# Optimization experiments

Measured on AMD Instinct MI355X. Metric: run time of the kernel, lower is better.

Reference implementation:

```python
import jax, jax.numpy as jnp
import numpy as np

B, S, D, H = 8, 8192, 256, 256


def setup_inputs() -> dict:
    key = jax.random.key(0)
    ks = jax.random.split(key, 5)
    scale = 1.0 / np.sqrt(D)  # mimic nn.Linear init scale
    return {
        "x": jax.random.normal(ks[0], (B, S, D), dtype=jnp.float32),
        "h0": jnp.zeros((B, 1, H), dtype=jnp.float32),
        "w_h_w": jax.random.normal(ks[1], (H, D), dtype=jnp.float32) * scale,
        "w_h_b": jax.random.normal(ks[2], (H,), dtype=jnp.float32) * scale,
        "w_z_w": jax.random.normal(ks[3], (H, D), dtype=jnp.float32) * scale,
        "w_z_b": jax.random.normal(ks[4], (H,), dtype=jnp.float32) * scale,
    }


def reference(x, h0, w_h_w, w_h_b, w_z_w, w_z_b):
    # Projections over the whole sequence (same math as per-step Linear calls)
    z = jax.nn.sigmoid(jnp.einsum('bsd,hd->bsh', x, w_z_w) + w_z_b)  # [B,S,H]
    h_tilde = jnp.einsum('bsd,hd->bsh', x, w_h_w) + w_h_b            # [B,S,H]

    def step(h_prev, zh):
        z_t, ht_t = zh  # each [B,H]
        h_t = (1.0 - z_t) * h_prev + z_t * ht_t
        return h_t, h_t

    # scan over time axis; carry is [B,H]
    _, hs = jax.lax.scan(step, h0[:, 0],
                         (jnp.swapaxes(z, 0, 1), jnp.swapaxes(h_tilde, 0, 1)))
    return jnp.swapaxes(hs, 0, 1)  # [B,S,H]
```

## Files before the change

### kernel.cpp

```cpp
#include <hip/hip_runtime.h>
#include <math.h>


constexpr int B_ = 8;
constexpr int S_ = 8192;
constexpr int D_ = 256;
constexpr int H_ = 256;
constexpr int M_ = B_ * S_;
constexpr int CHUNKS = 128;
constexpr int CLEN = S_ / CHUNKS;

typedef __attribute__((ext_vector_type(8))) short bf16x8;
typedef __attribute__((ext_vector_type(4))) float f32x4;

__device__ __forceinline__ uint pack2bf(float f0, float f1) {
  const uint u0 = __float_as_uint(f0) + 0x8000u;
  const uint u1 = __float_as_uint(f1) + 0x8000u;
  return __builtin_amdgcn_perm(u1, u0, 0x07060302u);
}

__device__ __forceinline__ float a_of(uint u) { return __uint_as_float(u << 16); }
__device__ __forceinline__ float b_of(uint u) { return __uint_as_float(u & 0xFFFF0000u); }

__global__ __launch_bounds__(256) void prep_w(
    const float* __restrict__ wzw, const float* __restrict__ whw,
    uint4* __restrict__ wb)
{
  const int u = blockIdx.x * 256 + threadIdx.x;
  const int proj = u >> 13;
  const float* s = (proj ? whw : wzw) + (size_t)(u & 8191) * 8;
  wb[u] = make_uint4(pack2bf(s[0], s[1]), pack2bf(s[2], s[3]),
                     pack2bf(s[4], s[5]), pack2bf(s[6], s[7]));
}

__global__ __launch_bounds__(512, 4) void gemm_zh(
    const float* __restrict__ x, const ushort* __restrict__ wbu,
    const float* __restrict__ whb, const float* __restrict__ wzb,
    uint* __restrict__ ab, float2* __restrict__ chunkPQ)
{
  __shared__ ushort xs[128][72];
  __shared__ ushort wzs[128][72];
  __shared__ ushort whs[128][72];

  const int tid = threadIdx.x;
  const int g    = blockIdx.x;
  const int xcd  = g & 7;
  const int loc  = g >> 3;
  const int nt   = loc & 1;
  const int panel = (loc >> 1) * 8 + xcd;
  const int m0 = panel * 128;
  const int n0 = nt * 128;

  const int lane = tid & 63;
  const int w  = tid >> 6;
  const int mb = (w & 1) * 64;
  const int nb = (w >> 1) * 32;
  const int q  = lane >> 4;
  const int cn = lane & 15;

  f32x4 accz[4][2] = {};
  f32x4 acch[4][2] = {};

  for (int k0 = 0; k0 < D_; k0 += 64) {
    __syncthreads();
#pragma unroll
    for (int f = 0; f < 4; f++) {
      const int idx = tid + 512 * f;
      const int row = idx >> 4, seg = idx & 15;
      float4 v = *(const float4*)(x + (size_t)(m0 + row) * D_ + k0 + seg * 4);
      *(uint2*)&xs[row][seg * 4] =
          make_uint2(pack2bf(v.x, v.y), pack2bf(v.z, v.w));
    }
#pragma unroll
    for (int f = 0; f < 4; f++) {
      const int idx = tid + 512 * f;
      const int proj = idx >> 10;
      const int r   = (idx >> 3) & 127, seg = idx & 7;
      const uint4 v = *(const uint4*)(wbu + (size_t)proj * H_ * D_ +
                                      (size_t)(n0 + r) * D_ + k0 + seg * 8);
      ushort* dst = proj ? &whs[r][seg * 8] : &wzs[r][seg * 8];
      *(uint4*)dst = v;
    }
    __syncthreads();
#pragma unroll
    for (int ks = 0; ks < 2; ks++) {
      const int kk = ks * 32 + q * 8;
      bf16x8 af[4], bz[2], bh[2];
#pragma unroll
      for (int i = 0; i < 4; i++)
        af[i] = *(const bf16x8*)&xs[mb + i * 16 + cn][kk];
#pragma unroll
      for (int j = 0; j < 2; j++) {
        bz[j] = *(const bf16x8*)&wzs[nb + j * 16 + cn][kk];
        bh[j] = *(const bf16x8*)&whs[nb + j * 16 + cn][kk];
      }
#pragma unroll
      for (int i = 0; i < 4; i++)
#pragma unroll
        for (int j = 0; j < 2; j++) {
          accz[i][j] = __builtin_amdgcn_mfma_f32_16x16x32_bf16(af[i], bz[j], accz[i][j], 0, 0, 0);
          acch[i][j] = __builtin_amdgcn_mfma_f32_16x16x32_bf16(af[i], bh[j], acch[i][j], 0, 0, 0);
        }
    }
  }

  const int row0 = m0 + mb;
  const int bb2  = row0 >> 13;
  const int cc   = (row0 & 8191) >> 6;

#pragma unroll
  for (int j = 0; j < 2; j++) {
    const int ch = n0 + nb + j * 16 + cn;
    const float zb = wzb[ch], hb = whb[ch];
    uint u[4][4];
#pragma unroll
    for (int i = 0; i < 4; i++) {
#pragma unroll
      for (int r = 0; r < 4; r++) {
        const int row = m0 + mb + i * 16 + q * 4 + r;
        const float zpre = accz[i][j][r] + zb;
        const float hpre = acch[i][j][r] + hb;
        const float e = __expf(-zpre);
        const float rcp = __builtin_amdgcn_rcpf(1.0f + e);
        const uint pk = pack2bf(e * rcp, hpre * rcp);
        ab[(size_t)row * H_ + ch] = pk;
        u[i][r] = pk;
      }
    }
    float P[4], Q[4];
#pragma unroll
    for (int i = 0; i < 4; i++) {
      float Pi = 1.f, Qi = 0.f;
#pragma unroll
      for (int r = 0; r < 4; r++) {
        const float a  = a_of(u[i][r]);
        const float bv = b_of(u[i][r]);
        Qi = fmaf(a, Qi, bv);
        Pi *= a;
      }
      P[i] = Pi; Q[i] = Qi;
    }
#pragma unroll
    for (int i = 0; i < 4; i++) {
      {
        const float Pp = __shfl_xor(P[i], 16);
        const float Qp = __shfl_xor(Q[i], 16);
        const bool later = (lane & 16) != 0;
        Q[i] = later ? fmaf(P[i], Qp, Q[i]) : fmaf(Pp, Q[i], Qp);
        P[i] = P[i] * Pp;
      }
      {
        const float Pp = __shfl_xor(P[i], 32);
        const float Qp = __shfl_xor(Q[i], 32);
        const bool later = (lane & 32) != 0;
        Q[i] = later ? fmaf(P[i], Qp, Q[i]) : fmaf(Pp, Q[i], Qp);
        P[i] = P[i] * Pp;
      }
    }
    float Pc = P[0], Qc = Q[0];
#pragma unroll
    for (int i = 1; i < 4; i++) {
      Qc = fmaf(P[i], Qc, Q[i]);
      Pc *= P[i];
    }
    if (lane < 16)
      chunkPQ[((size_t)bb2 * CHUNKS + cc) * H_ + ch] = make_float2(Pc, Qc);
  }
}

__global__ __launch_bounds__(256) void scan_phaseB(
    const float* __restrict__ h0in, const float2* __restrict__ pq,
    float* __restrict__ hstate)
{
  const int b = blockIdx.x;
  const int h = threadIdx.x;
  const size_t base = (size_t)b * CHUNKS * H_ + h;
  float hc = h0in[(size_t)b * H_ + h];
  for (int c0 = 0; c0 < CHUNKS; c0 += 16) {
    float2 v[16];
#pragma unroll
    for (int j = 0; j < 16; j++)
      v[j] = pq[base + (size_t)(c0 + j) * H_];
#pragma unroll
    for (int j = 0; j < 16; j++) {
      hstate[base + (size_t)(c0 + j) * H_] = hc;
      hc = fmaf(v[j].x, hc, v[j].y);
    }
  }
}

__global__ __launch_bounds__(64) void scan_phaseC(
    const uint* __restrict__ ab, const float* __restrict__ hstate,
    float* __restrict__ out)
{
  const int cid = blockIdx.x;
  const int b = cid >> 7;
  const int c = cid & (CHUNKS - 1);
  const int ch4 = threadIdx.x * 4;
  const size_t ebase = ((size_t)b * S_ + (size_t)c * CLEN) * H_ + ch4;

  float4 h4 = *(const float4*)(hstate + ((size_t)b * CHUNKS + c) * H_ + ch4);
  float h0v = h4.x, h1v = h4.y, h2v = h4.z, h3v = h4.w;

#pragma unroll
  for (int t0 = 0; t0 < CLEN; t0 += 8) {
    uint4 v[8];
#pragma unroll
    for (int j = 0; j < 8; j++)
      v[j] = *(const uint4*)(ab + ebase + (size_t)(t0 + j) * H_);
#pragma unroll
    for (int j = 0; j < 8; j++) {
      float4 o;
      o.x = h0v = fmaf(a_of(v[j].x), h0v, b_of(v[j].x));
      o.y = h1v = fmaf(a_of(v[j].y), h1v, b_of(v[j].y));
      o.z = h2v = fmaf(a_of(v[j].z), h2v, b_of(v[j].z));
      o.w = h3v = fmaf(a_of(v[j].w), h3v, b_of(v[j].w));
      *(float4*)(out + ebase + (size_t)(t0 + j) * H_) = o;
    }
  }
}

extern "C" void kernel_launch(void* const* d_in, const int* in_sizes, int n_in,
                              void* d_out, int out_size, void* d_ws, size_t ws_size,
                              hipStream_t stream) {
  const float* x   = (const float*)d_in[0];
  const float* h0  = (const float*)d_in[1];
  const float* whw = (const float*)d_in[2];
  const float* whb = (const float*)d_in[3];
  const float* wzw = (const float*)d_in[4];
  const float* wzb = (const float*)d_in[5];
  float* out = (float*)d_out;

  uint*   ab      = (uint*)d_ws;
  float2* chunkPQ = (float2*)(ab + (size_t)M_ * H_);
  float*  hstate  = (float*)(chunkPQ + (size_t)B_ * CHUNKS * H_);
  ushort* wb      = (ushort*)(hstate + (size_t)B_ * CHUNKS * H_);

  prep_w<<<64, 256, 0, stream>>>(wzw, whw, (uint4*)wb);
  gemm_zh<<<(M_ / 128) * (H_ / 128), 512, 0, stream>>>(
      x, wb, whb, wzb, ab, chunkPQ);
  scan_phaseB<<<B_, 256, 0, stream>>>(h0, (const float2*)chunkPQ, hstate);
  scan_phaseC<<<B_ * CHUNKS, 64, 0, stream>>>(ab, hstate, out);
}
```

Baseline: 177.2 us.

## Split scan phase C into four sub-chunks using per-sub-chunk carry products

The GEMM epilogue now also stores the per-16-row (P,Q) partial composites for each 64-step chunk. Phase C launches four wavefronts per chunk: each one first advances the chunk's starting state through the preceding sub-chunks, then scans only its own 16 timesteps. This cuts the serial dependency length per thread by four and raises parallelism in the memory-bound final pass. The cost is an extra partial-product buffer written by the GEMM and read by phase C, plus a few extra FMAs per thread.

```diff
diff --git a/kernel.cpp b/kernel.cpp
--- a/kernel.cpp
+++ b/kernel.cpp
@@ -36,7 +36,8 @@
 __global__ __launch_bounds__(512, 4) void gemm_zh(
     const float* __restrict__ x, const ushort* __restrict__ wbu,
     const float* __restrict__ whb, const float* __restrict__ wzb,
-    uint* __restrict__ ab, float2* __restrict__ chunkPQ)
+    uint* __restrict__ ab, float2* __restrict__ chunkPQ,
+    float2* __restrict__ pqsub)
 {
   __shared__ ushort xs[128][72];
   __shared__ ushort wzs[128][72];
@@ -112,9 +113,10 @@
   for (int j = 0; j < 2; j++) {
     const int ch = n0 + nb + j * 16 + cn;
     const float zb = wzb[ch], hb = whb[ch];
-    uint u[4][4];
+    float P[4], Q[4];
 #pragma unroll
     for (int i = 0; i < 4; i++) {
+      float Pi = 1.f, Qi = 0.f;
 #pragma unroll
       for (int r = 0; r < 4; r++) {
         const int row = m0 + mb + i * 16 + q * 4 + r;
@@ -124,17 +126,8 @@
         const float rcp = __builtin_amdgcn_rcpf(1.0f + e);
         const uint pk = pack2bf(e * rcp, hpre * rcp);
         ab[(size_t)row * H_ + ch] = pk;
-        u[i][r] = pk;
-      }
-    }
-    float P[4], Q[4];
-#pragma unroll
-    for (int i = 0; i < 4; i++) {
-      float Pi = 1.f, Qi = 0.f;
-#pragma unroll
-      for (int r = 0; r < 4; r++) {
-        const float a  = a_of(u[i][r]);
-        const float bv = b_of(u[i][r]);
+        const float a  = a_of(pk);
+        const float bv = b_of(pk);
         Qi = fmaf(a, Qi, bv);
         Pi *= a;
       }
@@ -163,8 +156,13 @@
       Qc = fmaf(P[i], Qc, Q[i]);
       Pc *= P[i];
     }
-    if (lane < 16)
+    if (lane < 16) {
+      const size_t sb = ((size_t)bb2 * CHUNKS + cc) * 4;
+#pragma unroll
+      for (int i = 0; i < 4; i++)
+        pqsub[(sb + i) * H_ + ch] = make_float2(P[i], Q[i]);
       chunkPQ[((size_t)bb2 * CHUNKS + cc) * H_ + ch] = make_float2(Pc, Qc);
+    }
   }
 }
 
@@ -189,21 +187,38 @@
   }
 }
 
-__global__ __launch_bounds__(64) void scan_phaseC(
+__global__ __launch_bounds__(256) void scan_phaseC(
     const uint* __restrict__ ab, const float* __restrict__ hstate,
-    float* __restrict__ out)
+    const float2* __restrict__ pqsub, float* __restrict__ out)
 {
   const int cid = blockIdx.x;
   const int b = cid >> 7;
   const int c = cid & (CHUNKS - 1);
-  const int ch4 = threadIdx.x * 4;
-  const size_t ebase = ((size_t)b * S_ + (size_t)c * CLEN) * H_ + ch4;
+  const int g = threadIdx.x >> 6;
+  const int ch4 = (threadIdx.x & 63) * 4;
 
   float4 h4 = *(const float4*)(hstate + ((size_t)b * CHUNKS + c) * H_ + ch4);
   float h0v = h4.x, h1v = h4.y, h2v = h4.z, h3v = h4.w;
 
-#pragma unroll
-  for (int t0 = 0; t0 < CLEN; t0 += 8) {
+  const float2* ps = pqsub + ((size_t)b * CHUNKS + c) * 4 * H_ + ch4;
+#pragma unroll
+  for (int k = 0; k < 3; k++) {
+    if (k < g) {
+      const float2 p0 = ps[(size_t)k * H_ + 0];
+      const float2 p1 = ps[(size_t)k * H_ + 1];
+      const float2 p2 = ps[(size_t)k * H_ + 2];
+      const float2 p3 = ps[(size_t)k * H_ + 3];
+      h0v = fmaf(p0.x, h0v, p0.y);
+      h1v = fmaf(p1.x, h1v, p1.y);
+      h2v = fmaf(p2.x, h2v, p2.y);
+      h3v = fmaf(p3.x, h3v, p3.y);
+    }
+  }
+
+  const size_t ebase =
+      ((size_t)b * S_ + (size_t)c * CLEN + g * 16) * H_ + ch4;
+#pragma unroll
+  for (int t0 = 0; t0 < 16; t0 += 8) {
     uint4 v[8];
 #pragma unroll
     for (int j = 0; j < 8; j++)
@@ -233,12 +248,13 @@
 
   uint*   ab      = (uint*)d_ws;
   float2* chunkPQ = (float2*)(ab + (size_t)M_ * H_);
-  float*  hstate  = (float*)(chunkPQ + (size_t)B_ * CHUNKS * H_);
+  float2* pqsub   = chunkPQ + (size_t)B_ * CHUNKS * H_;
+  float*  hstate  = (float*)(pqsub + (size_t)B_ * CHUNKS * 4 * H_);
   ushort* wb      = (ushort*)(hstate + (size_t)B_ * CHUNKS * H_);
 
   prep_w<<<64, 256, 0, stream>>>(wzw, whw, (uint4*)wb);
   gemm_zh<<<(M_ / 128) * (H_ / 128), 512, 0, stream>>>(
-      x, wb, whb, wzb, ab, chunkPQ);
+      x, wb, whb, wzb, ab, chunkPQ, pqsub);
   scan_phaseB<<<B_, 256, 0, stream>>>(h0, (const float2*)chunkPQ, hstate);
-  scan_phaseC<<<B_ * CHUNKS, 64, 0, stream>>>(ab, hstate, out);
-}
+  scan_phaseC<<<B_ * CHUNKS, 256, 0, stream>>>(ab, hstate, pqsub, out);
+}
```

After: 180.2 us. About the same (+1.7%).

## Recompute GEMM in output pass instead of storing packed gate/candidate buffer

Applied to the files above, without the earlier changes.

Removes the intermediate bf16-packed (a,b) buffer. The first GEMM pass now only produces per-chunk scan summaries, and a second GEMM pass recomputes the projections and applies the chunk-local scan directly from registers using the carried-in state. This trades a 64 MB write plus read of the intermediate for re-reading x (32 MB) and redoing the matmul. The in-register scan adds shuffle-based prefix combination across lane groups.

```diff
diff --git a/kernel.cpp b/kernel.cpp
--- a/kernel.cpp
+++ b/kernel.cpp
@@ -33,110 +33,96 @@
                      pack2bf(s[4], s[5]), pack2bf(s[6], s[7]));
 }
 
-__global__ __launch_bounds__(512, 4) void gemm_zh(
+#define GEMM_PREAMBLE(xptr, wptr)                                            \
+  __shared__ ushort xs[128][72];                                             \
+  __shared__ ushort wzs[128][72];                                            \
+  __shared__ ushort whs[128][72];                                            \
+  const int tid = threadIdx.x;                                               \
+  const int g    = blockIdx.x;                                               \
+  const int xcd  = g & 7;                                                    \
+  const int loc  = g >> 3;                                                   \
+  const int nt   = loc & 1;                                                  \
+  const int panel = (loc >> 1) * 8 + xcd;                                    \
+  const int m0 = panel * 128;                                                \
+  const int n0 = nt * 128;                                                   \
+  const int lane = tid & 63;                                                 \
+  const int w  = tid >> 6;                                                   \
+  const int mb = (w & 1) * 64;                                               \
+  const int nb = (w >> 1) * 32;                                              \
+  const int q  = lane >> 4;                                                  \
+  const int cn = lane & 15;                                                  \
+  f32x4 accz[4][2] = {};                                                     \
+  f32x4 acch[4][2] = {};                                                     \
+  for (int k0 = 0; k0 < D_; k0 += 64) {                                      \
+    __syncthreads();                                                         \
+    _Pragma("unroll")                                                        \
+    for (int f = 0; f < 4; f++) {                                            \
+      const int idx = tid + 512 * f;                                         \
+      const int row = idx >> 4, seg = idx & 15;                              \
+      float4 v = *(const float4*)(xptr + (size_t)(m0 + row) * D_ + k0 + seg * 4); \
+      *(uint2*)&xs[row][seg * 4] =                                           \
+          make_uint2(pack2bf(v.x, v.y), pack2bf(v.z, v.w));                  \
+    }                                                                        \
+    _Pragma("unroll")                                                        \
+    for (int f = 0; f < 4; f++) {                                            \
+      const int idx = tid + 512 * f;                                         \
+      const int proj = idx >> 10;                                            \
+      const int r   = (idx >> 3) & 127, seg = idx & 7;                       \
+      const uint4 v = *(const uint4*)(wptr + (size_t)proj * H_ * D_ +        \
+                                      (size_t)(n0 + r) * D_ + k0 + seg * 8); \
+      ushort* dst = proj ? &whs[r][seg * 8] : &wzs[r][seg * 8];              \
+      *(uint4*)dst = v;                                                      \
+    }                                                                        \
+    __syncthreads();                                                         \
+    _Pragma("unroll")                                                        \
+    for (int ks = 0; ks < 2; ks++) {                                         \
+      const int kk = ks * 32 + q * 8;                                        \
+      bf16x8 af[4], bz[2], bh[2];                                            \
+      _Pragma("unroll")                                                      \
+      for (int i = 0; i < 4; i++)                                            \
+        af[i] = *(const bf16x8*)&xs[mb + i * 16 + cn][kk];                   \
+      _Pragma("unroll")                                                      \
+      for (int j = 0; j < 2; j++) {                                          \
+        bz[j] = *(const bf16x8*)&wzs[nb + j * 16 + cn][kk];                  \
+        bh[j] = *(const bf16x8*)&whs[nb + j * 16 + cn][kk];                  \
+      }                                                                      \
+      _Pragma("unroll")                                                      \
+      for (int i = 0; i < 4; i++)                                            \
+        _Pragma("unroll")                                                    \
+        for (int j = 0; j < 2; j++) {                                        \
+          accz[i][j] = __builtin_amdgcn_mfma_f32_16x16x32_bf16(af[i], bz[j], accz[i][j], 0, 0, 0); \
+          acch[i][j] = __builtin_amdgcn_mfma_f32_16x16x32_bf16(af[i], bh[j], acch[i][j], 0, 0, 0); \
+        }                                                                    \
+    }                                                                        \
+  }                                                                          \
+  const int row0 = m0 + mb;                                                  \
+  const int bb2  = row0 >> 13;                                               \
+  const int cc   = (row0 & 8191) >> 6;
+
+__global__ __launch_bounds__(512, 4) void gemm_sum(
     const float* __restrict__ x, const ushort* __restrict__ wbu,
     const float* __restrict__ whb, const float* __restrict__ wzb,
-    uint* __restrict__ ab, float2* __restrict__ chunkPQ)
-{
-  __shared__ ushort xs[128][72];
-  __shared__ ushort wzs[128][72];
-  __shared__ ushort whs[128][72];
-
-  const int tid = threadIdx.x;
-  const int g    = blockIdx.x;
-  const int xcd  = g & 7;
-  const int loc  = g >> 3;
-  const int nt   = loc & 1;
-  const int panel = (loc >> 1) * 8 + xcd;
-  const int m0 = panel * 128;
-  const int n0 = nt * 128;
-
-  const int lane = tid & 63;
-  const int w  = tid >> 6;
-  const int mb = (w & 1) * 64;
-  const int nb = (w >> 1) * 32;
-  const int q  = lane >> 4;
-  const int cn = lane & 15;
-
-  f32x4 accz[4][2] = {};
-  f32x4 acch[4][2] = {};
-
-  for (int k0 = 0; k0 < D_; k0 += 64) {
-    __syncthreads();
-#pragma unroll
-    for (int f = 0; f < 4; f++) {
-      const int idx = tid + 512 * f;
-      const int row = idx >> 4, seg = idx & 15;
-      float4 v = *(const float4*)(x + (size_t)(m0 + row) * D_ + k0 + seg * 4);
-      *(uint2*)&xs[row][seg * 4] =
-          make_uint2(pack2bf(v.x, v.y), pack2bf(v.z, v.w));
-    }
-#pragma unroll
-    for (int f = 0; f < 4; f++) {
-      const int idx = tid + 512 * f;
-      const int proj = idx >> 10;
-      const int r   = (idx >> 3) & 127, seg = idx & 7;
-      const uint4 v = *(const uint4*)(wbu + (size_t)proj * H_ * D_ +
-                                      (size_t)(n0 + r) * D_ + k0 + seg * 8);
-      ushort* dst = proj ? &whs[r][seg * 8] : &wzs[r][seg * 8];
-      *(uint4*)dst = v;
-    }
-    __syncthreads();
-#pragma unroll
-    for (int ks = 0; ks < 2; ks++) {
-      const int kk = ks * 32 + q * 8;
-      bf16x8 af[4], bz[2], bh[2];
-#pragma unroll
-      for (int i = 0; i < 4; i++)
-        af[i] = *(const bf16x8*)&xs[mb + i * 16 + cn][kk];
-#pragma unroll
-      for (int j = 0; j < 2; j++) {
-        bz[j] = *(const bf16x8*)&wzs[nb + j * 16 + cn][kk];
-        bh[j] = *(const bf16x8*)&whs[nb + j * 16 + cn][kk];
-      }
-#pragma unroll
-      for (int i = 0; i < 4; i++)
-#pragma unroll
-        for (int j = 0; j < 2; j++) {
-          accz[i][j] = __builtin_amdgcn_mfma_f32_16x16x32_bf16(af[i], bz[j], accz[i][j], 0, 0, 0);
-          acch[i][j] = __builtin_amdgcn_mfma_f32_16x16x32_bf16(af[i], bh[j], acch[i][j], 0, 0, 0);
-        }
-    }
-  }
-
-  const int row0 = m0 + mb;
-  const int bb2  = row0 >> 13;
-  const int cc   = (row0 & 8191) >> 6;
+    float2* __restrict__ chunkPQ)
+{
+  GEMM_PREAMBLE(x, wbu)
 
 #pragma unroll
   for (int j = 0; j < 2; j++) {
     const int ch = n0 + nb + j * 16 + cn;
     const float zb = wzb[ch], hb = whb[ch];
-    uint u[4][4];
-#pragma unroll
-    for (int i = 0; i < 4; i++) {
+    float P[4], Q[4];
+#pragma unroll
+    for (int i = 0; i < 4; i++) {
+      float Pi = 1.f, Qi = 0.f;
 #pragma unroll
       for (int r = 0; r < 4; r++) {
-        const int row = m0 + mb + i * 16 + q * 4 + r;
         const float zpre = accz[i][j][r] + zb;
         const float hpre = acch[i][j][r] + hb;
         const float e = __expf(-zpre);
         const float rcp = __builtin_amdgcn_rcpf(1.0f + e);
         const uint pk = pack2bf(e * rcp, hpre * rcp);
-        ab[(size_t)row * H_ + ch] = pk;
-        u[i][r] = pk;
-      }
-    }
-    float P[4], Q[4];
-#pragma unroll
-    for (int i = 0; i < 4; i++) {
-      float Pi = 1.f, Qi = 0.f;
-#pragma unroll
-      for (int r = 0; r < 4; r++) {
-        const float a  = a_of(u[i][r]);
-        const float bv = b_of(u[i][r]);
-        Qi = fmaf(a, Qi, bv);
-        Pi *= a;
+        Qi = fmaf(a_of(pk), Qi, b_of(pk));
+        Pi *= a_of(pk);
       }
       P[i] = Pi; Q[i] = Qi;
     }
@@ -189,33 +175,64 @@
   }
 }
 
-__global__ __launch_bounds__(64) void scan_phaseC(
-    const uint* __restrict__ ab, const float* __restrict__ hstate,
-    float* __restrict__ out)
-{
-  const int cid = blockIdx.x;
-  const int b = cid >> 7;
-  const int c = cid & (CHUNKS - 1);
-  const int ch4 = threadIdx.x * 4;
-  const size_t ebase = ((size_t)b * S_ + (size_t)c * CLEN) * H_ + ch4;
-
-  float4 h4 = *(const float4*)(hstate + ((size_t)b * CHUNKS + c) * H_ + ch4);
-  float h0v = h4.x, h1v = h4.y, h2v = h4.z, h3v = h4.w;
-
-#pragma unroll
-  for (int t0 = 0; t0 < CLEN; t0 += 8) {
-    uint4 v[8];
-#pragma unroll
-    for (int j = 0; j < 8; j++)
-      v[j] = *(const uint4*)(ab + ebase + (size_t)(t0 + j) * H_);
-#pragma unroll
-    for (int j = 0; j < 8; j++) {
-      float4 o;
-      o.x = h0v = fmaf(a_of(v[j].x), h0v, b_of(v[j].x));
-      o.y = h1v = fmaf(a_of(v[j].y), h1v, b_of(v[j].y));
-      o.z = h2v = fmaf(a_of(v[j].z), h2v, b_of(v[j].z));
-      o.w = h3v = fmaf(a_of(v[j].w), h3v, b_of(v[j].w));
-      *(float4*)(out + ebase + (size_t)(t0 + j) * H_) = o;
+__global__ __launch_bounds__(512, 4) void gemm_out(
+    const float* __restrict__ x, const ushort* __restrict__ wbu,
+    const float* __restrict__ whb, const float* __restrict__ wzb,
+    const float* __restrict__ hstate, float* __restrict__ out)
+{
+  GEMM_PREAMBLE(x, wbu)
+
+#pragma unroll
+  for (int j = 0; j < 2; j++) {
+    const int ch = n0 + nb + j * 16 + cn;
+    const float zb = wzb[ch], hb = whb[ch];
+    uint u[4][4];
+    float P[4], Q[4];
+#pragma unroll
+    for (int i = 0; i < 4; i++) {
+      float Pi = 1.f, Qi = 0.f;
+#pragma unroll
+      for (int r = 0; r < 4; r++) {
+        const float zpre = accz[i][j][r] + zb;
+        const float hpre = acch[i][j][r] + hb;
+        const float e = __expf(-zpre);
+        const float rcp = __builtin_amdgcn_rcpf(1.0f + e);
+        const uint pk = pack2bf(e * rcp, hpre * rcp);
+        u[i][r] = pk;
+        Qi = fmaf(a_of(pk), Qi, b_of(pk));
+        Pi *= a_of(pk);
+      }
+      P[i] = Pi; Q[i] = Qi;
+    }
+#pragma unroll
+    for (int i = 0; i < 4; i++) {
+#pragma unroll
+      for (int d = 1; d <= 2; d++) {
+        const int src = (q >= d) ? (lane - 16 * d) : lane;
+        const float Pp = __shfl(P[i], src);
+        const float Qp = __shfl(Q[i], src);
+        if (q >= d) {
+          Q[i] = fmaf(P[i], Qp, Q[i]);
+          P[i] = P[i] * Pp;
+        }
+      }
+    }
+    float hst = hstate[((size_t)bb2 * CHUNKS + cc) * H_ + ch];
+#pragma unroll
+    for (int i = 0; i < 4; i++) {
+      const float Tp = __shfl(P[i], cn + 48);
+      const float Tq = __shfl(Q[i], cn + 48);
+      const float Ps = __shfl(P[i], (q > 0) ? (lane - 16) : lane);
+      const float Qs = __shfl(Q[i], (q > 0) ? (lane - 16) : lane);
+      const float Pe = (q == 0) ? 1.f : Ps;
+      const float Qe = (q == 0) ? 0.f : Qs;
+      float hcur = fmaf(Pe, hst, Qe);
+#pragma unroll
+      for (int r = 0; r < 4; r++) {
+        hcur = fmaf(a_of(u[i][r]), hcur, b_of(u[i][r]));
+        out[(size_t)(m0 + mb + i * 16 + q * 4 + r) * H_ + ch] = hcur;
+      }
+      hst = fmaf(Tp, hst, Tq);
     }
   }
 }
@@ -231,14 +248,14 @@
   const float* wzb = (const float*)d_in[5];
   float* out = (float*)d_out;
 
-  uint*   ab      = (uint*)d_ws;
-  float2* chunkPQ = (float2*)(ab + (size_t)M_ * H_);
+  float2* chunkPQ = (float2*)d_ws;
   float*  hstate  = (float*)(chunkPQ + (size_t)B_ * CHUNKS * H_);
   ushort* wb      = (ushort*)(hstate + (size_t)B_ * CHUNKS * H_);
 
   prep_w<<<64, 256, 0, stream>>>(wzw, whw, (uint4*)wb);
-  gemm_zh<<<(M_ / 128) * (H_ / 128), 512, 0, stream>>>(
-      x, wb, whb, wzb, ab, chunkPQ);
+  gemm_sum<<<(M_ / 128) * (H_ / 128), 512, 0, stream>>>(
+      x, wb, whb, wzb, chunkPQ);
   scan_phaseB<<<B_, 256, 0, stream>>>(h0, (const float2*)chunkPQ, hstate);
-  scan_phaseC<<<B_ * CHUNKS, 64, 0, stream>>>(ab, hstate, out);
-}
+  gemm_out<<<(M_ / 128) * (H_ / 128), 512, 0, stream>>>(
+      x, wb, whb, wzb, hstate, out);
+}
```

Result: no change. 176.7 us (-0.3%).
